# Kernel tuning notes

Hardware: AMD Instinct MI355X
Metric: run time of the kernel (lower is better)

The kernel has to match this reference:

```python
import jax, jax.numpy as jnp
from jax import lax
import numpy as np

B, H, W, D_MODEL = 2, 64, 64, 192
D_INNER, D_STATE, DT_RANK = 384, 16, 12
L = H * W
LN_EPS = 1e-5


def setup_inputs() -> dict:
    ks = jax.random.split(jax.random.key(0), 12)
    rng = np.random.default_rng(0)
    perm = rng.permutation(L).astype(np.int32)

    def p(i, shape, scale=0.02):
        return jax.random.normal(ks[i], shape, dtype=jnp.float32) * scale

    return {
        "x": jax.random.normal(ks[0], (B, H, W, D_MODEL), dtype=jnp.float32),
        "condition": jax.random.normal(ks[1], (B, H, W, D_MODEL), dtype=jnp.float32),
        "W_in": p(2, (2 * D_INNER, D_MODEL)),
        "W_con": p(3, (D_INNER, D_MODEL)),
        "conv_w": p(4, (D_INNER, 1, 3, 3)),
        "conv_b": jnp.zeros((D_INNER,), jnp.float32),
        "con_conv_w": p(5, (D_INNER, 1, 3, 3)),
        "con_conv_b": jnp.zeros((D_INNER,), jnp.float32),
        "x_proj_w": p(6, (DT_RANK + 2 * D_STATE, D_INNER)),
        "dt_proj_w": p(7, (D_INNER, DT_RANK)),
        "dt_proj_b": p(8, (D_INNER,), 0.1),
        "A_logs": jnp.tile(jnp.log(jnp.arange(1, D_STATE + 1, dtype=jnp.float32))[None, :], (D_INNER, 1)),
        "Ds": jnp.ones((D_INNER,), jnp.float32),
        "ln_w": jnp.ones((D_INNER,), jnp.float32),
        "ln_b": jnp.zeros((D_INNER,), jnp.float32),
        "W_out": p(9, (D_MODEL, D_INNER)),
        "scan_path": jnp.asarray(perm),
        "rev_scan_path": jnp.asarray(np.argsort(perm).astype(np.int32)),
    }


def _dwconv(x, w, b):
    # depthwise 3x3 conv, SAME padding; x: [B, C, H, W], w: [C, 1, 3, 3]
    y = lax.conv_general_dilated(x, w, (1, 1), "SAME",
                                 dimension_numbers=("NCHW", "OIHW", "NCHW"),
                                 feature_group_count=x.shape[1])
    return y + b[None, :, None, None]


def _selective_scan(u, delta, A, Bs, Cs, D):
    # u, delta: [B, D, L]; A: [D, N]; Bs, Cs: [B, N, L]; D: [D]
    dA = jnp.exp(jnp.einsum("bdl,dn->lbdn", delta, A))          # [L, B, D, N]
    dBu = jnp.einsum("bdl,bnl,bdl->lbdn", delta, Bs, u)          # [L, B, D, N]
    Ct = jnp.transpose(Cs, (2, 0, 1))                             # [L, B, N]
    h0 = jnp.zeros(dA.shape[1:], dA.dtype)

    def step(h, inp):
        a, b, c = inp
        h = a * h + b
        return h, jnp.einsum("bdn,bn->bd", h, c)

    _, ys = lax.scan(step, h0, (dA, dBu, Ct))                     # ys: [L, B, D]
    y = jnp.transpose(ys, (1, 2, 0))                              # [B, D, L]
    return y + u * D[None, :, None]


def _forward(x, condition, W_in, W_con, conv_w, conv_b, con_conv_w, con_conv_b,
             x_proj_w, dt_proj_w, dt_proj_b, A_logs, Ds, ln_w, ln_b, W_out,
             scan_path, rev_scan_path):
    b, h, w, _ = x.shape
    l = h * w
    xz = x @ W_in.T                                               # [B, H, W, 2*Din]
    xa, z = jnp.split(xz, 2, axis=-1)
    z = jax.nn.silu(z)
    c = condition @ W_con.T
    xa = jax.nn.silu(_dwconv(jnp.transpose(xa, (0, 3, 1, 2)), conv_w, conv_b))
    c = jax.nn.silu(_dwconv(jnp.transpose(c, (0, 3, 1, 2)), con_conv_w, con_conv_b))
    d = xa.shape[1]
    xs = xa.reshape(b, d, l)[:, :, scan_path]                     # forward_permutation, K=1
    cs = c.reshape(b, d, l)[:, :, scan_path]
    x_dbl = jnp.einsum("bdl,cd->bcl", xs + cs, x_proj_w)          # [B, R+2N, L]
    r, n = dt_proj_w.shape[1], A_logs.shape[1]
    dts = jnp.einsum("brl,dr->bdl", x_dbl[:, :r], dt_proj_w)
    Bs = x_dbl[:, r:r + n]
    Cs = x_dbl[:, r + n:]
    A = -jnp.exp(A_logs)
    delta = jax.nn.softplus(dts + dt_proj_b[None, :, None])       # delta_softplus=True
    y = _selective_scan(xs, delta, A, Bs, Cs, Ds)                 # [B, D, L]
    y = y[:, :, rev_scan_path]                                    # backward_permutation
    y = jnp.transpose(y, (0, 2, 1))                               # [B, L, D]
    mu = jnp.mean(y, axis=-1, keepdims=True)
    var = jnp.var(y, axis=-1, keepdims=True)
    y = (y - mu) * lax.rsqrt(var + LN_EPS) * ln_w + ln_b          # out_norm
    y = y.reshape(b, h, w, d) * z
    return y @ W_out.T                                            # out_proj (no bias)


def reference(x, condition, W_in, W_con, conv_w, conv_b, con_conv_w, con_conv_b,
              x_proj_w, dt_proj_w, dt_proj_b, A_logs, Ds, ln_w, ln_b, W_out,
              scan_path, rev_scan_path):
    return _forward(x, condition, W_in, W_con, conv_w, conv_b, con_conv_w,
                    con_conv_b, x_proj_w, dt_proj_w, dt_proj_b, A_logs, Ds,
                    ln_w, ln_b, W_out, scan_path, rev_scan_path)
```

## Files before the change

kernel.cpp:

```cpp
#include <hip/hip_runtime.h>
#include <math.h>

#define BB 2
#define HH 64
#define WW 64
#define DM 192
#define DI 384
#define NS 16
#define DTR 12
#define LL 4096
#define ROWS (BB*LL)
#define NCHUNK 128
#define LCHUNK 32
#define NCOMB 448
#define CSTRIDE ((size_t)BB * DI * 8)

typedef __attribute__((ext_vector_type(8))) short bf16x8;
typedef __attribute__((ext_vector_type(4))) float f32x4;

typedef __attribute__((address_space(3))) void        as3_void;
typedef __attribute__((address_space(1))) const void  as1_cvoid;

__device__ __forceinline__ void gl_lds16(const unsigned short* g, unsigned short* l) {
    __builtin_amdgcn_global_load_lds((as1_cvoid*)g, (as3_void*)l, 16, 0, 0);
}

#define WAITCNT_BARRIER(N)                                         \
    do {                                                           \
        asm volatile("s_waitcnt vmcnt(" #N ")" ::: "memory");      \
        __builtin_amdgcn_s_barrier();                              \
        asm volatile("" ::: "memory");                             \
    } while (0)

__device__ __forceinline__ float silu_f(float v) {
    return v / (1.0f + __expf(-v));
}

__device__ __forceinline__ unsigned short f2bf(float f) {
    union { float f; unsigned int u; } c; c.f = f;
    unsigned int u = c.u;
    u += 0x7fffu + ((u >> 16) & 1u);
    return (unsigned short)(u >> 16);
}
__device__ __forceinline__ float bf2f(unsigned short h) {
    union { unsigned int u; float f; } c; c.u = ((unsigned int)h) << 16;
    return c.f;
}

__device__ __forceinline__ bf16x8 f2bf8(float4 a, float4 b) {
    bf16x8 r;
    r[0] = (short)f2bf(a.x); r[1] = (short)f2bf(a.y);
    r[2] = (short)f2bf(a.z); r[3] = (short)f2bf(a.w);
    r[4] = (short)f2bf(b.x); r[5] = (short)f2bf(b.y);
    r[6] = (short)f2bf(b.z); r[7] = (short)f2bf(b.w);
    return r;
}

__global__ __launch_bounds__(256) void gemm_in(
    const float* __restrict__ x, const float* __restrict__ cond,
    const float* __restrict__ w_in, const float* __restrict__ w_con,
    const float* __restrict__ x_proj_w, const float* __restrict__ dt_w,
    const float* __restrict__ w_out,
    unsigned short* __restrict__ xa_bf, unsigned short* __restrict__ z_bf,
    unsigned short* __restrict__ c_bf,
    unsigned short* __restrict__ wcomb_bf, unsigned short* __restrict__ w_out_bf)
{
    const int y = blockIdx.y;
    __shared__ __align__(16) unsigned short sA[2 * 64 * 32];
    __shared__ __align__(16) unsigned short sB[2 * 64 * 32];

    if (y == 18) {
        const int base = blockIdx.x * 256 + threadIdx.x;
        for (int i = base; i < 18432; i += 32768) {
            float4 v = ((const float4*)w_out)[i];
            ushort4 o;
            o.x = f2bf(v.x); o.y = f2bf(v.y); o.z = f2bf(v.z); o.w = f2bf(v.w);
            ((ushort4*)w_out_bf)[i] = o;
        }
        for (int e = base; e < NCOMB * DI; e += 32768) {
            int row = e / DI, k = e - row * DI;
            float v = 0.f;
            if (row < 384) {
                const float* dw = dt_w + row * DTR;
                #pragma unroll
                for (int r = 0; r < DTR; ++r) v += dw[r] * x_proj_w[r * DI + k];
            } else if (row < 416) {
                v = x_proj_w[(12 + (row - 384)) * DI + k];
            }
            wcomb_bf[e] = f2bf(v);
        }
        return;
    }

    const int zz = (y >= 12) ? 1 : 0;
    const float* A = zz ? cond : x;
    const float* W = zz ? w_con : w_in;
    const int bn = (zz ? (y - 12) : y) * 64;
    const int bm = blockIdx.x * 64;

    const int tid  = threadIdx.x;
    const int wave = tid >> 6;
    const int lane = tid & 63;
    const int quad = lane >> 4;
    const int l16  = lane & 15;
    const int srow = tid >> 2;
    const int q4   = tid & 3;
    const int wcol = (q4 ^ ((srow >> 1) & 3)) * 8;
    const int rswz = (quad ^ ((l16 >> 1) & 3)) * 8;

    f32x4 acc[4];
    #pragma unroll
    for (int t = 0; t < 4; ++t) acc[t] = (f32x4)(0.f);

    const float* gA = &A[(size_t)(bm + srow) * DM + q4 * 8];
    const float* gB = &W[(size_t)(bn + srow) * DM + q4 * 8];

    float4 ra0 = *(const float4*)gA,        ra1 = *(const float4*)(gA + 4);
    float4 rb0 = *(const float4*)gB,        rb1 = *(const float4*)(gB + 4);
    *(bf16x8*)&sA[srow * 32 + wcol] = f2bf8(ra0, ra1);
    *(bf16x8*)&sB[srow * 32 + wcol] = f2bf8(rb0, rb1);
    ra0 = *(const float4*)(gA + 32); ra1 = *(const float4*)(gA + 36);
    rb0 = *(const float4*)(gB + 32); rb1 = *(const float4*)(gB + 36);

    const int ar = (wave * 16 + l16) * 32 + rswz;

    #pragma unroll
    for (int t = 0; t < 6; ++t) {
        __syncthreads();
        const unsigned short* cA = &sA[(t & 1) * 2048];
        const unsigned short* cB = &sB[(t & 1) * 2048];
        bf16x8 a = *(bf16x8*)&cA[ar];
        if (t + 1 < 6) {
            const int nb = (t + 1) & 1;
            *(bf16x8*)&sA[nb * 2048 + srow * 32 + wcol] = f2bf8(ra0, ra1);
            *(bf16x8*)&sB[nb * 2048 + srow * 32 + wcol] = f2bf8(rb0, rb1);
            if (t + 2 < 6) {
                const int k = (t + 2) * 32;
                ra0 = *(const float4*)(gA + k); ra1 = *(const float4*)(gA + k + 4);
                rb0 = *(const float4*)(gB + k); rb1 = *(const float4*)(gB + k + 4);
            }
        }
        #pragma unroll
        for (int n = 0; n < 4; ++n) {
            bf16x8 b = *(bf16x8*)&cB[(n * 16 + l16) * 32 + rswz];
            acc[n] = __builtin_amdgcn_mfma_f32_16x16x32_bf16(a, b, acc[n], 0, 0, 0);
        }
    }

    #pragma unroll
    for (int n = 0; n < 4; ++n) {
        int col = bn + n * 16 + l16;
        #pragma unroll
        for (int r = 0; r < 4; ++r) {
            int row = bm + wave * 16 + quad * 4 + r;
            float v = acc[n][r];
            if (zz == 0) {
                if (col < 384) xa_bf[(size_t)row * 384 + col] = f2bf(v);
                else           z_bf[(size_t)row * 384 + (col - 384)] = f2bf(silu_f(v));
            } else {
                c_bf[(size_t)row * 384 + col] = f2bf(v);
            }
        }
    }
}

__global__ __launch_bounds__(256) void gemm_comb(
    const unsigned short* __restrict__ A, const unsigned short* __restrict__ W,
    const float* __restrict__ bias, float* __restrict__ btct,
    unsigned short* __restrict__ du_lo)
{
    __shared__ __align__(16) unsigned short sA[4 * 64 * 32];
    __shared__ __align__(16) unsigned short sB[4 * 64 * 32];
    const int bm = blockIdx.x * 64;
    const int bn = blockIdx.y * 64;
    const int tid  = threadIdx.x;
    const int wave = tid >> 6;
    const int lane = tid & 63;
    const int quad = lane >> 4;
    const int l16  = lane & 15;
    const int srow = tid >> 2;
    const int scol = ((tid & 3) ^ ((tid >> 3) & 3)) * 8;
    const int rswz = (quad ^ ((l16 >> 1) & 3)) * 8;

    f32x4 acc[4];
    #pragma unroll
    for (int t = 0; t < 4; ++t) acc[t] = (f32x4)(0.f);

    const unsigned short* gA = &A[(size_t)(bm + srow) * DI + scol];
    const unsigned short* gB = &W[(size_t)(bn + srow) * DI + scol];

    #pragma unroll
    for (int p = 0; p < 3; ++p) {
        gl_lds16(gA + p * 32, &sA[p * 2048 + wave * 512]);
        gl_lds16(gB + p * 32, &sB[p * 2048 + wave * 512]);
    }
    WAITCNT_BARRIER(4);

    const int ar = (wave * 16 + l16) * 32 + rswz;

    #pragma unroll
    for (int t = 0; t < 12; ++t) {
        if (t + 3 < 12) {
            const int k = (t + 3) * 32, pb = (t + 3) & 3;
            gl_lds16(gA + k, &sA[pb * 2048 + wave * 512]);
            gl_lds16(gB + k, &sB[pb * 2048 + wave * 512]);
        }
        const unsigned short* cA = &sA[(t & 3) * 2048];
        const unsigned short* cB = &sB[(t & 3) * 2048];
        bf16x8 a = *(bf16x8*)&cA[ar];
        #pragma unroll
        for (int n = 0; n < 4; ++n) {
            bf16x8 b = *(bf16x8*)&cB[(n * 16 + l16) * 32 + rswz];
            acc[n] = __builtin_amdgcn_mfma_f32_16x16x32_bf16(a, b, acc[n], 0, 0, 0);
        }
        if (t < 11) {
            if (t + 3 < 12)      WAITCNT_BARRIER(4);
            else if (t + 2 < 12) WAITCNT_BARRIER(2);
            else                 WAITCNT_BARRIER(0);
        }
    }

    #pragma unroll
    for (int n = 0; n < 4; ++n) {
        int col = bn + n * 16 + l16;
        #pragma unroll
        for (int r = 0; r < 4; ++r) {
            int row = bm + wave * 16 + quad * 4 + r;
            float v = acc[n][r];
            if (col < 384) {
                float a = v + bias[col];
                float sp = (a > 20.f) ? a : log1pf(__expf(a));
                du_lo[((size_t)row * 384 + col) * 2] = f2bf(sp);
            } else if (col < 416) {
                int idx = col - 384;
                int pos = (idx < 16) ? ((idx & 7) * 4 + (idx >> 3))
                                     : (((idx - 16) & 7) * 4 + 2 + ((idx - 16) >> 3));
                btct[(size_t)row * 32 + pos] = v;
            }
        }
    }
}

__global__ __launch_bounds__(256) void gemm_out_fused(
    const unsigned short* __restrict__ yt, const unsigned short* __restrict__ z,
    const int* __restrict__ rev_path,
    const float* __restrict__ ln_w, const float* __restrict__ ln_b,
    const unsigned short* __restrict__ W, float* __restrict__ out)
{
    __shared__ __align__(16) unsigned short sA[32 * 392];
    __shared__ __align__(16) unsigned short sB[3 * 64 * 32];
    const int bm = blockIdx.x * 32;
    const int bn = blockIdx.y * 64;
    const int tid = threadIdx.x;
    const int r2  = tid >> 3;
    const int q8  = tid & 7;
    const int b   = bm >> 12;
    const int l   = (bm & (LL - 1)) + r2;
    const int js  = rev_path[l];

    const unsigned short* yrow = yt + ((size_t)(b * LL + js)) * DI;
    const unsigned short* zrow = z  + ((size_t)(b * LL + l)) * DI;

    bf16x8 yv[6];
    float s = 0.f, s2 = 0.f;
    #pragma unroll
    for (int i = 0; i < 6; ++i) {
        yv[i] = *(const bf16x8*)&yrow[i * 64 + q8 * 8];
        #pragma unroll
        for (int e = 0; e < 8; ++e) {
            float f = bf2f((unsigned short)yv[i][e]);
            s += f; s2 += f * f;
        }
    }
    s  += __shfl_xor(s, 1);  s  += __shfl_xor(s, 2);  s  += __shfl_xor(s, 4);
    s2 += __shfl_xor(s2, 1); s2 += __shfl_xor(s2, 2); s2 += __shfl_xor(s2, 4);
    const float mu  = s * (1.0f / DI);
    const float inv = rsqrtf(s2 * (1.0f / DI) - mu * mu + 1e-5f);

    #pragma unroll
    for (int i = 0; i < 6; ++i) {
        int c = i * 64 + q8 * 8;
        bf16x8 zv = *(const bf16x8*)&zrow[c];
        float4 wa = *(const float4*)&ln_w[c];
        float4 wb = *(const float4*)&ln_w[c + 4];
        float4 ba = *(const float4*)&ln_b[c];
        float4 bb = *(const float4*)&ln_b[c + 4];
        bf16x8 o;
        o[0] = (short)f2bf(((bf2f((unsigned short)yv[i][0]) - mu) * inv * wa.x + ba.x) * bf2f((unsigned short)zv[0]));
        o[1] = (short)f2bf(((bf2f((unsigned short)yv[i][1]) - mu) * inv * wa.y + ba.y) * bf2f((unsigned short)zv[1]));
        o[2] = (short)f2bf(((bf2f((unsigned short)yv[i][2]) - mu) * inv * wa.z + ba.z) * bf2f((unsigned short)zv[2]));
        o[3] = (short)f2bf(((bf2f((unsigned short)yv[i][3]) - mu) * inv * wa.w + ba.w) * bf2f((unsigned short)zv[3]));
        o[4] = (short)f2bf(((bf2f((unsigned short)yv[i][4]) - mu) * inv * wb.x + bb.x) * bf2f((unsigned short)zv[4]));
        o[5] = (short)f2bf(((bf2f((unsigned short)yv[i][5]) - mu) * inv * wb.y + bb.y) * bf2f((unsigned short)zv[5]));
        o[6] = (short)f2bf(((bf2f((unsigned short)yv[i][6]) - mu) * inv * wb.z + bb.z) * bf2f((unsigned short)zv[6]));
        o[7] = (short)f2bf(((bf2f((unsigned short)yv[i][7]) - mu) * inv * wb.w + bb.w) * bf2f((unsigned short)zv[7]));
        *(bf16x8*)&sA[r2 * 392 + c] = o;
    }

    const int wave = tid >> 6;
    const int lane = tid & 63;
    const int quad = lane >> 4;
    const int l16  = lane & 15;
    const int srow = tid >> 2;
    const int scol = ((tid & 3) ^ ((tid >> 3) & 3)) * 8;
    const int rswz = (quad ^ ((l16 >> 1) & 3)) * 8;
    const int rf   = wave >> 1;
    const int np   = (wave & 1) * 2;

    f32x4 acc[2];
    acc[0] = (f32x4)(0.f); acc[1] = (f32x4)(0.f);

    const unsigned short* gB = &W[(size_t)(bn + srow) * DI + scol];
    const int abase = (rf * 16 + l16) * 392 + quad * 8;

    gl_lds16(gB,      &sB[0 * 2048 + wave * 512]);
    gl_lds16(gB + 32, &sB[1 * 2048 + wave * 512]);
    __syncthreads();

    #pragma unroll
    for (int t = 0; t < 12; ++t) {
        if (t + 2 < 12)
            gl_lds16(gB + (t + 2) * 32, &sB[((t + 2) % 3) * 2048 + wave * 512]);
        bf16x8 a = *(bf16x8*)&sA[abase + t * 32];
        const unsigned short* cB = &sB[(t % 3) * 2048];
        #pragma unroll
        for (int k = 0; k < 2; ++k) {
            bf16x8 bfr = *(bf16x8*)&cB[((np + k) * 16 + l16) * 32 + rswz];
            acc[k] = __builtin_amdgcn_mfma_f32_16x16x32_bf16(a, bfr, acc[k], 0, 0, 0);
        }
        if (t < 11) {
            if (t + 2 < 12) WAITCNT_BARRIER(1);
            else            WAITCNT_BARRIER(0);
        }
    }

    #pragma unroll
    for (int k = 0; k < 2; ++k) {
        int col = bn + (np + k) * 16 + l16;
        #pragma unroll
        for (int rr = 0; rr < 4; ++rr) {
            int row = bm + rf * 16 + quad * 4 + rr;
            out[(size_t)row * DM + col] = acc[k][rr];
        }
    }
}

__global__ __launch_bounds__(256) void dwconv2_scatter(
    const unsigned short* __restrict__ xin, const unsigned short* __restrict__ cin,
    const float* __restrict__ wx, const float* __restrict__ bx,
    const float* __restrict__ wc, const float* __restrict__ bc,
    const int* __restrict__ rev_scan_path,
    unsigned short* __restrict__ du_hi,
    unsigned short* __restrict__ s_bf)
{
    const int tile = blockIdx.x;
    const int c0   = blockIdx.y * 32;
    const int b    = blockIdx.z;
    const int h0 = (tile >> 3) * 8, w0 = (tile & 7) * 8;
    __shared__ float smx[10 * 10 * 32];
    __shared__ float smc[10 * 10 * 32];
    __shared__ int   jtile[64];

    for (int idx = threadIdx.x; idx < 800; idx += 256) {
        int pix = idx >> 3, cq = (idx & 7) * 4;
        int py = pix / 10, px = pix - py * 10;
        int gh = h0 + py - 1, gw = w0 + px - 1;
        float4 fx = make_float4(0.f, 0.f, 0.f, 0.f);
        float4 fc = make_float4(0.f, 0.f, 0.f, 0.f);
        if (gh >= 0 && gh < 64 && gw >= 0 && gw < 64) {
            size_t g = ((size_t)(b * LL + gh * 64 + gw)) * DI + c0 + cq;
            ushort4 vx = *(const ushort4*)&xin[g];
            ushort4 vc = *(const ushort4*)&cin[g];
            fx = make_float4(bf2f(vx.x), bf2f(vx.y), bf2f(vx.z), bf2f(vx.w));
            fc = make_float4(bf2f(vc.x), bf2f(vc.y), bf2f(vc.z), bf2f(vc.w));
        }
        *(float4*)&smx[pix * 32 + cq] = fx;
        *(float4*)&smc[pix * 32 + cq] = fc;
    }
    if (threadIdx.x < 64) {
        int l = (h0 + (threadIdx.x >> 3)) * 64 + (w0 + (threadIdx.x & 7));
        jtile[threadIdx.x] = rev_scan_path[l];
    }
    __syncthreads();

    const int ch = threadIdx.x & 31;
    const int pq = threadIdx.x >> 5;
    float wrx[9], wrc[9];
    #pragma unroll
    for (int k = 0; k < 9; ++k) {
        wrx[k] = wx[(c0 + ch) * 9 + k];
        wrc[k] = wc[(c0 + ch) * 9 + k];
    }
    const float bvx = bx[c0 + ch];
    const float bvc = bc[c0 + ch];

    #pragma unroll
    for (int i = 0; i < 8; ++i) {
        int p  = pq * 8 + i;
        int ph = p >> 3, pw = p & 7;
        float ax = bvx, ac = bvc;
        #pragma unroll
        for (int ki = 0; ki < 3; ++ki)
            #pragma unroll
            for (int kj = 0; kj < 3; ++kj) {
                int si = ((ph + ki) * 10 + (pw + kj)) * 32 + ch;
                ax += wrx[ki * 3 + kj] * smx[si];
                ac += wrc[ki * 3 + kj] * smc[si];
            }
        float xv = silu_f(ax);
        float sv = xv + silu_f(ac);
        size_t o = ((size_t)(b * LL + jtile[p])) * DI + c0 + ch;
        du_hi[o * 2 + 1] = f2bf(xv);
        s_bf[o]          = f2bf(sv);
    }
}

__global__ __launch_bounds__(256) void scan_chunkA(
    const unsigned int* __restrict__ du, const float* __restrict__ btct,
    const float* __restrict__ A_logs,
    float* __restrict__ chunkA, float* __restrict__ chunkB)
{
    const int c = blockIdx.x;
    const int g = blockIdx.y;
    const int b = blockIdx.z;
    const int t = threadIdx.x;
    const int grp = t >> 3, p = t & 7;
    const int d = g * 32 + grp;
    const float Av0 = -__expf(A_logs[d * NS + p]);
    const float Av1 = -__expf(A_logs[d * NS + p + 8]);
    const int j0 = c * LCHUNK;

    const unsigned int* dul = du + ((size_t)b * LL + j0) * DI + d;
    const float2*       bl  = (const float2*)btct + ((size_t)b * LL + j0) * 16 + p * 2;

    float h0 = 0.f, h1 = 0.f, Sd = 0.f;
    unsigned int duv[4]; float2 bv[4];
    #pragma unroll
    for (int q = 0; q < 4; ++q) {
        duv[q] = dul[(size_t)q * DI]; bv[q] = bl[(size_t)q * 16];
    }
    for (int j = 0; j < LCHUNK; j += 4) {
        unsigned int ndu[4]; float2 nb[4];
        if (j + 4 < LCHUNK) {
            #pragma unroll
            for (int q = 0; q < 4; ++q) {
                int jj = j + 4 + q;
                ndu[q] = dul[(size_t)jj * DI]; nb[q] = bl[(size_t)jj * 16];
            }
        }
        #pragma unroll
        for (int q = 0; q < 4; ++q) {
            float dv = bf2f((unsigned short)(duv[q] & 0xffff));
            float uv = bf2f((unsigned short)(duv[q] >> 16));
            float e0 = __expf(dv * Av0);
            float e1 = __expf(dv * Av1);
            float duu = dv * uv;
            h0 = e0 * h0 + bv[q].x * duu;
            h1 = e1 * h1 + bv[q].y * duu;
            Sd += dv;
        }
        #pragma unroll
        for (int q = 0; q < 4; ++q) { duv[q]=ndu[q]; bv[q]=nb[q]; }
    }
    size_t idx = (size_t)c * CSTRIDE + ((size_t)b * DI + d) * 8 + p;
    ((float2*)chunkA)[idx] = make_float2(__expf(Sd * Av0), __expf(Sd * Av1));
    ((float2*)chunkB)[idx] = make_float2(h0, h1);
}

__global__ __launch_bounds__(256) void scan_chunkC(
    const unsigned int* __restrict__ du, const float* __restrict__ btct,
    const float* __restrict__ A_logs, const float* __restrict__ Ds,
    const float* __restrict__ chunkA, const float* __restrict__ chunkB,
    unsigned short* __restrict__ yt)
{
    const int c = blockIdx.x;
    const int g = blockIdx.y;
    const int b = blockIdx.z;
    const int t = threadIdx.x;
    const int grp = t >> 3, p = t & 7;
    const int d = g * 32 + grp;
    const float Av0 = -__expf(A_logs[d * NS + p]);
    const float Av1 = -__expf(A_logs[d * NS + p + 8]);
    const float Dv = Ds[d];
    const int j0 = c * LCHUNK;

    const unsigned int* dul = du + ((size_t)b * LL + j0) * DI + d;
    const float4*       bcl = (const float4*)btct + ((size_t)b * LL + j0) * 8 + p;
    unsigned short* yl = yt + ((size_t)b * LL + j0) * DI + d;

    const size_t off = ((size_t)b * DI + d) * 8 + p;
    const float2* A2 = (const float2*)chunkA;
    const float2* B2 = (const float2*)chunkB;
    float h0 = 0.f, h1 = 0.f, P0 = 1.f, P1 = 1.f;
    for (int i = c - 1; i >= 0; --i) {
        size_t ix = (size_t)i * CSTRIDE + off;
        float2 a = A2[ix], bv = B2[ix];
        h0 += P0 * bv.x;  h1 += P1 * bv.y;
        P0 *= a.x;        P1 *= a.y;
        if (fmaxf(fabsf(P0), fabsf(P1)) < 1e-30f) break;
    }

    unsigned int duv[4]; float4 bc[4];
    #pragma unroll
    for (int q = 0; q < 4; ++q) {
        duv[q] = dul[(size_t)q * DI]; bc[q] = bcl[(size_t)q * 8];
    }
    for (int j = 0; j < LCHUNK; j += 4) {
        unsigned int ndu[4]; float4 nbc[4];
        if (j + 4 < LCHUNK) {
            #pragma unroll
            for (int q = 0; q < 4; ++q) {
                int jj = j + 4 + q;
                ndu[q] = dul[(size_t)jj * DI]; nbc[q] = bcl[(size_t)jj * 8];
            }
        }
        #pragma unroll
        for (int q = 0; q < 4; ++q) {
            float dv = bf2f((unsigned short)(duv[q] & 0xffff));
            float uv = bf2f((unsigned short)(duv[q] >> 16));
            float e0 = __expf(dv * Av0);
            float e1 = __expf(dv * Av1);
            float duu = dv * uv;
            h0 = e0 * h0 + bc[q].x * duu;
            h1 = e1 * h1 + bc[q].y * duu;
            float acc = h0 * bc[q].z + h1 * bc[q].w;
            acc += __shfl_xor(acc, 4, 8);
            acc += __shfl_xor(acc, 2, 8);
            acc += __shfl_xor(acc, 1, 8);
            if (p == 0) yl[(size_t)(j + q) * DI] = f2bf(acc + uv * Dv);
        }
        #pragma unroll
        for (int q = 0; q < 4; ++q) { duv[q]=ndu[q]; bc[q]=nbc[q]; }
    }
}

extern "C" void kernel_launch(void* const* d_in, const int* in_sizes, int n_in,
                              void* d_out, int out_size, void* d_ws, size_t ws_size,
                              hipStream_t stream) {
    const float* x          = (const float*)d_in[0];
    const float* cond       = (const float*)d_in[1];
    const float* W_in       = (const float*)d_in[2];
    const float* W_con      = (const float*)d_in[3];
    const float* conv_w     = (const float*)d_in[4];
    const float* conv_b     = (const float*)d_in[5];
    const float* con_conv_w = (const float*)d_in[6];
    const float* con_conv_b = (const float*)d_in[7];
    const float* x_proj_w   = (const float*)d_in[8];
    const float* dt_proj_w  = (const float*)d_in[9];
    const float* dt_proj_b  = (const float*)d_in[10];
    const float* A_logs     = (const float*)d_in[11];
    const float* Ds         = (const float*)d_in[12];
    const float* ln_w       = (const float*)d_in[13];
    const float* ln_b       = (const float*)d_in[14];
    const float* W_out      = (const float*)d_in[15];
    const int*   scan_path  = (const int*)d_in[16];
    const int*   rev_path   = (const int*)d_in[17];
    (void)scan_path;

    float* ws = (float*)d_ws;
    const size_t S  = (size_t)BB * LL * DI;
    const size_t SC = (size_t)NCHUNK * BB * DI * NS;
    float* ytslab  = ws + 0 * S;
    float* zslab   = ws + 1 * S;
    float* duslab  = ws + 2 * S;
    float* btct    = ws + 3 * S;
    float* chunkA  = btct + (size_t)BB * LL * 32;
    float* chunkB  = chunkA + SC;
    float* bfpool  = chunkB + SC;

    unsigned short* yt_bf    = (unsigned short*)ytslab;
    unsigned short* z_bf     = (unsigned short*)zslab;
    unsigned int*   du       = (unsigned int*)duslab;
    unsigned short* s_bf     = (unsigned short*)bfpool;
    unsigned short* xa_bf    = s_bf + (size_t)ROWS * DI;
    unsigned short* c_bf     = xa_bf + (size_t)ROWS * DI;
    unsigned short* w_out_bf = c_bf + (size_t)ROWS * DI;
    unsigned short* wcomb_bf = w_out_bf + 192 * DI;

    gemm_in<<<dim3(ROWS / 64, 19), 256, 0, stream>>>(
        x, cond, W_in, W_con, x_proj_w, dt_proj_w, W_out,
        xa_bf, z_bf, c_bf, wcomb_bf, w_out_bf);
    dwconv2_scatter<<<dim3(64, 12, BB), 256, 0, stream>>>(
        xa_bf, c_bf, conv_w, conv_b, con_conv_w, con_conv_b,
        rev_path, (unsigned short*)du, s_bf);
    gemm_comb<<<dim3(ROWS / 64, NCOMB / 64), 256, 0, stream>>>(
        s_bf, wcomb_bf, dt_proj_b, btct, (unsigned short*)du);
    scan_chunkA<<<dim3(NCHUNK, DI / 32, BB), 256, 0, stream>>>(
        du, btct, A_logs, chunkA, chunkB);
    scan_chunkC<<<dim3(NCHUNK, DI / 32, BB), 256, 0, stream>>>(
        du, btct, A_logs, Ds, chunkA, chunkB, yt_bf);
    gemm_out_fused<<<dim3(ROWS / 32, DM / 64), 256, 0, stream>>>(
        yt_bf, z_bf, rev_path, ln_w, ln_b, w_out_bf, (float*)d_out);
}
```

Baseline: 196.9 us.

## Keep full-K A panel in LDS and loop over N tiles in gemm_in

gemm_in now loads a 32-row slab of the fp32 activation, converts it to bf16 once into a swizzled full-K LDS panel, and then loops over all N tiles (12 for W_in, 6 for W_con) within one block, streaming B tiles. Previously each of the 18 column-tile blocks re-read and re-converted the same A rows. The grid shrinks from 128x19 to 256x3 blocks. In exchange, each block does serial work across N tiles with per-tile syncs and fewer MFMAs per wave per tile, so parallelism and latency hiding are reduced.

```diff
diff --git a/kernel.cpp b/kernel.cpp
--- a/kernel.cpp
+++ b/kernel.cpp
@@ -66,18 +66,18 @@
     unsigned short* __restrict__ wcomb_bf, unsigned short* __restrict__ w_out_bf)
 {
     const int y = blockIdx.y;
-    __shared__ __align__(16) unsigned short sA[2 * 64 * 32];
+    __shared__ __align__(16) unsigned short sAp[32 * 192];
     __shared__ __align__(16) unsigned short sB[2 * 64 * 32];
 
-    if (y == 18) {
+    if (y == 2) {
         const int base = blockIdx.x * 256 + threadIdx.x;
-        for (int i = base; i < 18432; i += 32768) {
+        for (int i = base; i < 18432; i += 65536) {
             float4 v = ((const float4*)w_out)[i];
             ushort4 o;
             o.x = f2bf(v.x); o.y = f2bf(v.y); o.z = f2bf(v.z); o.w = f2bf(v.w);
             ((ushort4*)w_out_bf)[i] = o;
         }
-        for (int e = base; e < NCOMB * DI; e += 32768) {
+        for (int e = base; e < NCOMB * DI; e += 65536) {
             int row = e / DI, k = e - row * DI;
             float v = 0.f;
             if (row < 384) {
@@ -92,11 +92,11 @@
         return;
     }
 
-    const int zz = (y >= 12) ? 1 : 0;
+    const int zz = y;
     const float* A = zz ? cond : x;
     const float* W = zz ? w_con : w_in;
-    const int bn = (zz ? (y - 12) : y) * 64;
-    const int bm = blockIdx.x * 64;
+    const int ntiles = zz ? 6 : 12;
+    const int bm = blockIdx.x * 32;
 
     const int tid  = threadIdx.x;
     const int wave = tid >> 6;
@@ -107,58 +107,72 @@
     const int q4   = tid & 3;
     const int wcol = (q4 ^ ((srow >> 1) & 3)) * 8;
     const int rswz = (quad ^ ((l16 >> 1) & 3)) * 8;
-
-    f32x4 acc[4];
-    #pragma unroll
-    for (int t = 0; t < 4; ++t) acc[t] = (f32x4)(0.f);
-
-    const float* gA = &A[(size_t)(bm + srow) * DM + q4 * 8];
-    const float* gB = &W[(size_t)(bn + srow) * DM + q4 * 8];
-
-    float4 ra0 = *(const float4*)gA,        ra1 = *(const float4*)(gA + 4);
-    float4 rb0 = *(const float4*)gB,        rb1 = *(const float4*)(gB + 4);
-    *(bf16x8*)&sA[srow * 32 + wcol] = f2bf8(ra0, ra1);
-    *(bf16x8*)&sB[srow * 32 + wcol] = f2bf8(rb0, rb1);
-    ra0 = *(const float4*)(gA + 32); ra1 = *(const float4*)(gA + 36);
-    rb0 = *(const float4*)(gB + 32); rb1 = *(const float4*)(gB + 36);
-
-    const int ar = (wave * 16 + l16) * 32 + rswz;
-
-    #pragma unroll
-    for (int t = 0; t < 6; ++t) {
-        __syncthreads();
-        const unsigned short* cA = &sA[(t & 1) * 2048];
-        const unsigned short* cB = &sB[(t & 1) * 2048];
-        bf16x8 a = *(bf16x8*)&cA[ar];
-        if (t + 1 < 6) {
-            const int nb = (t + 1) & 1;
-            *(bf16x8*)&sA[nb * 2048 + srow * 32 + wcol] = f2bf8(ra0, ra1);
-            *(bf16x8*)&sB[nb * 2048 + srow * 32 + wcol] = f2bf8(rb0, rb1);
-            if (t + 2 < 6) {
-                const int k = (t + 2) * 32;
-                ra0 = *(const float4*)(gA + k); ra1 = *(const float4*)(gA + k + 4);
-                rb0 = *(const float4*)(gB + k); rb1 = *(const float4*)(gB + k + 4);
-            }
-        }
-        #pragma unroll
-        for (int n = 0; n < 4; ++n) {
-            bf16x8 b = *(bf16x8*)&cB[(n * 16 + l16) * 32 + rswz];
-            acc[n] = __builtin_amdgcn_mfma_f32_16x16x32_bf16(a, b, acc[n], 0, 0, 0);
-        }
-    }
-
-    #pragma unroll
-    for (int n = 0; n < 4; ++n) {
-        int col = bn + n * 16 + l16;
-        #pragma unroll
-        for (int r = 0; r < 4; ++r) {
-            int row = bm + wave * 16 + quad * 4 + r;
-            float v = acc[n][r];
-            if (zz == 0) {
-                if (col < 384) xa_bf[(size_t)row * 384 + col] = f2bf(v);
-                else           z_bf[(size_t)row * 384 + (col - 384)] = f2bf(silu_f(v));
-            } else {
-                c_bf[(size_t)row * 384 + col] = f2bf(v);
+    const int rf   = wave >> 1;
+    const int np   = (wave & 1) * 2;
+
+    {
+        const int ar = tid >> 3;
+        const int aj = tid & 7;
+        const float* gA = &A[(size_t)(bm + ar) * DM];
+        #pragma unroll
+        for (int s = 0; s < 3; ++s) {
+            int c = aj + s * 8;
+            float4 a0 = *(const float4*)(gA + c * 8);
+            float4 a1 = *(const float4*)(gA + c * 8 + 4);
+            int cc = (c & ~7) | ((c & 7) ^ (ar & 7));
+            *(bf16x8*)&sAp[ar * 192 + cc * 8] = f2bf8(a0, a1);
+        }
+    }
+
+    const int arow  = rf * 16 + l16;
+    const int abase = arow * 192;
+    const int axor  = arow & 7;
+
+    for (int nt = 0; nt < ntiles; ++nt) {
+        const int bn = nt * 64;
+        const float* gB = &W[(size_t)(bn + srow) * DM + q4 * 8];
+        f32x4 acc[2];
+        acc[0] = (f32x4)(0.f); acc[1] = (f32x4)(0.f);
+
+        float4 rb0 = *(const float4*)gB;
+        float4 rb1 = *(const float4*)(gB + 4);
+        *(bf16x8*)&sB[srow * 32 + wcol] = f2bf8(rb0, rb1);
+        rb0 = *(const float4*)(gB + 32); rb1 = *(const float4*)(gB + 36);
+
+        #pragma unroll
+        for (int t = 0; t < 6; ++t) {
+            __syncthreads();
+            const unsigned short* cB = &sB[(t & 1) * 2048];
+            const int chunk = t * 4 + quad;
+            const int cc = (chunk & ~7) | ((chunk & 7) ^ axor);
+            bf16x8 a = *(bf16x8*)&sAp[abase + cc * 8];
+            if (t + 1 < 6) {
+                *(bf16x8*)&sB[((t + 1) & 1) * 2048 + srow * 32 + wcol] = f2bf8(rb0, rb1);
+                if (t + 2 < 6) {
+                    rb0 = *(const float4*)(gB + (t + 2) * 32);
+                    rb1 = *(const float4*)(gB + (t + 2) * 32 + 4);
+                }
+            }
+            #pragma unroll
+            for (int k = 0; k < 2; ++k) {
+                bf16x8 b = *(bf16x8*)&cB[((np + k) * 16 + l16) * 32 + rswz];
+                acc[k] = __builtin_amdgcn_mfma_f32_16x16x32_bf16(a, b, acc[k], 0, 0, 0);
+            }
+        }
+
+        #pragma unroll
+        for (int k = 0; k < 2; ++k) {
+            int col = bn + (np + k) * 16 + l16;
+            #pragma unroll
+            for (int r = 0; r < 4; ++r) {
+                int row = bm + rf * 16 + quad * 4 + r;
+                float v = acc[k][r];
+                if (zz == 0) {
+                    if (col < 384) xa_bf[(size_t)row * 384 + col] = f2bf(v);
+                    else           z_bf[(size_t)row * 384 + (col - 384)] = f2bf(silu_f(v));
+                } else {
+                    c_bf[(size_t)row * 384 + col] = f2bf(v);
+                }
             }
         }
     }
@@ -577,7 +591,7 @@
     unsigned short* w_out_bf = c_bf + (size_t)ROWS * DI;
     unsigned short* wcomb_bf = w_out_bf + 192 * DI;
 
-    gemm_in<<<dim3(ROWS / 64, 19), 256, 0, stream>>>(
+    gemm_in<<<dim3(ROWS / 32, 3), 256, 0, stream>>>(
         x, cond, W_in, W_con, x_proj_w, dt_proj_w, W_out,
         xa_bf, z_bf, c_bf, wcomb_bf, w_out_bf);
     dwconv2_scatter<<<dim3(64, 12, BB), 256, 0, stream>>>(
```

New measurement: 213.3 us. +8.3%, slower.

## Scatter scan output via scan_path and load W_out fragments directly from global

Applied to the files above, without the earlier changes.

The scan kernel now writes each output row to its unpermuted position using scan_path, so the output GEMM reads y rows contiguously instead of gathering through rev_path. The output GEMM also drops its LDS triple-buffered async pipeline for W_out and loads B fragments straight from global memory, adding one barrier after the A staging. This removes the gather indirection and the per-step barriers, but makes the scan's stores scattered and makes B loads uncoalesced global reads that are not shared across waves.

```diff
diff --git a/kernel.cpp b/kernel.cpp
--- a/kernel.cpp
+++ b/kernel.cpp
@@ -243,12 +243,10 @@
 
 __global__ __launch_bounds__(256) void gemm_out_fused(
     const unsigned short* __restrict__ yt, const unsigned short* __restrict__ z,
-    const int* __restrict__ rev_path,
     const float* __restrict__ ln_w, const float* __restrict__ ln_b,
     const unsigned short* __restrict__ W, float* __restrict__ out)
 {
     __shared__ __align__(16) unsigned short sA[32 * 392];
-    __shared__ __align__(16) unsigned short sB[3 * 64 * 32];
     const int bm = blockIdx.x * 32;
     const int bn = blockIdx.y * 64;
     const int tid = threadIdx.x;
@@ -256,9 +254,8 @@
     const int q8  = tid & 7;
     const int b   = bm >> 12;
     const int l   = (bm & (LL - 1)) + r2;
-    const int js  = rev_path[l];
-
-    const unsigned short* yrow = yt + ((size_t)(b * LL + js)) * DI;
+
+    const unsigned short* yrow = yt + ((size_t)(b * LL + l)) * DI;
     const unsigned short* zrow = z  + ((size_t)(b * LL + l)) * DI;
 
     bf16x8 yv[6];
@@ -297,41 +294,29 @@
         *(bf16x8*)&sA[r2 * 392 + c] = o;
     }
 
+    __syncthreads();
+
     const int wave = tid >> 6;
     const int lane = tid & 63;
     const int quad = lane >> 4;
     const int l16  = lane & 15;
-    const int srow = tid >> 2;
-    const int scol = ((tid & 3) ^ ((tid >> 3) & 3)) * 8;
-    const int rswz = (quad ^ ((l16 >> 1) & 3)) * 8;
     const int rf   = wave >> 1;
     const int np   = (wave & 1) * 2;
 
     f32x4 acc[2];
     acc[0] = (f32x4)(0.f); acc[1] = (f32x4)(0.f);
 
-    const unsigned short* gB = &W[(size_t)(bn + srow) * DI + scol];
+    const unsigned short* bp0 = &W[(size_t)(bn + np * 16 + l16) * DI + quad * 8];
+    const unsigned short* bp1 = bp0 + (size_t)16 * DI;
     const int abase = (rf * 16 + l16) * 392 + quad * 8;
 
-    gl_lds16(gB,      &sB[0 * 2048 + wave * 512]);
-    gl_lds16(gB + 32, &sB[1 * 2048 + wave * 512]);
-    __syncthreads();
-
     #pragma unroll
     for (int t = 0; t < 12; ++t) {
-        if (t + 2 < 12)
-            gl_lds16(gB + (t + 2) * 32, &sB[((t + 2) % 3) * 2048 + wave * 512]);
-        bf16x8 a = *(bf16x8*)&sA[abase + t * 32];
-        const unsigned short* cB = &sB[(t % 3) * 2048];
-        #pragma unroll
-        for (int k = 0; k < 2; ++k) {
-            bf16x8 bfr = *(bf16x8*)&cB[((np + k) * 16 + l16) * 32 + rswz];
-            acc[k] = __builtin_amdgcn_mfma_f32_16x16x32_bf16(a, bfr, acc[k], 0, 0, 0);
-        }
-        if (t < 11) {
-            if (t + 2 < 12) WAITCNT_BARRIER(1);
-            else            WAITCNT_BARRIER(0);
-        }
+        bf16x8 a  = *(bf16x8*)&sA[abase + t * 32];
+        bf16x8 b0 = *(const bf16x8*)(bp0 + t * 32);
+        bf16x8 b1 = *(const bf16x8*)(bp1 + t * 32);
+        acc[0] = __builtin_amdgcn_mfma_f32_16x16x32_bf16(a, b0, acc[0], 0, 0, 0);
+        acc[1] = __builtin_amdgcn_mfma_f32_16x16x32_bf16(a, b1, acc[1], 0, 0, 0);
     }
 
     #pragma unroll
@@ -471,6 +456,7 @@
     const unsigned int* __restrict__ du, const float* __restrict__ btct,
     const float* __restrict__ A_logs, const float* __restrict__ Ds,
     const float* __restrict__ chunkA, const float* __restrict__ chunkB,
+    const int* __restrict__ scan_path,
     unsigned short* __restrict__ yt)
 {
     const int c = blockIdx.x;
@@ -486,7 +472,7 @@
 
     const unsigned int* dul = du + ((size_t)b * LL + j0) * DI + d;
     const float4*       bcl = (const float4*)btct + ((size_t)b * LL + j0) * 8 + p;
-    unsigned short* yl = yt + ((size_t)b * LL + j0) * DI + d;
+    unsigned short* ytb = yt + (size_t)b * LL * DI + d;
 
     const size_t off = ((size_t)b * DI + d) * 8 + p;
     const float2* A2 = (const float2*)chunkA;
@@ -527,7 +513,10 @@
             acc += __shfl_xor(acc, 4, 8);
             acc += __shfl_xor(acc, 2, 8);
             acc += __shfl_xor(acc, 1, 8);
-            if (p == 0) yl[(size_t)(j + q) * DI] = f2bf(acc + uv * Dv);
+            if (p == 0) {
+                int lsp = scan_path[j0 + j + q];
+                ytb[(size_t)lsp * DI] = f2bf(acc + uv * Dv);
+            }
         }
         #pragma unroll
         for (int q = 0; q < 4; ++q) { duv[q]=ndu[q]; bc[q]=nbc[q]; }
@@ -555,7 +544,6 @@
     const float* W_out      = (const float*)d_in[15];
     const int*   scan_path  = (const int*)d_in[16];
     const int*   rev_path   = (const int*)d_in[17];
-    (void)scan_path;
 
     float* ws = (float*)d_ws;
     const size_t S  = (size_t)BB * LL * DI;
@@ -588,7 +576,7 @@
     scan_chunkA<<<dim3(NCHUNK, DI / 32, BB), 256, 0, stream>>>(
         du, btct, A_logs, chunkA, chunkB);
     scan_chunkC<<<dim3(NCHUNK, DI / 32, BB), 256, 0, stream>>>(
-        du, btct, A_logs, Ds, chunkA, chunkB, yt_bf);
+        du, btct, A_logs, Ds, chunkA, chunkB, scan_path, yt_bf);
     gemm_out_fused<<<dim3(ROWS / 32, DM / 64), 256, 0, stream>>>(
-        yt_bf, z_bf, rev_path, ln_w, ln_b, w_out_bf, (float*)d_out);
-}
+        yt_bf, z_bf, ln_w, ln_b, w_out_bf, (float*)d_out);
+}
```

Result: no change. 197.9 us (+0.5%).
